# Optimization experiments

Hardware: AMD Instinct MI355X
Metric: run time of the kernel (lower is better)

## Reference

```python
import jax, jax.numpy as jnp
import numpy as np

C_IN, C_KEY, C_VAL, C_OUT = 256, 128, 128, 256
B, H, W = 4, 64, 64
BN_EPS = 1e-5


def conv1x1(x, w, b):
    # x: [B,C,H,W], w: [O,C], b: [O]
    return jnp.einsum('bchw,oc->bohw', x, w) + b[None, :, None, None]


def bn_relu(x, gamma, beta, mean, var):
    inv = jax.lax.rsqrt(var + BN_EPS)
    y = (x - mean[None, :, None, None]) * (gamma * inv)[None, :, None, None] + beta[None, :, None, None]
    return jax.nn.relu(y)


def setup_inputs() -> dict:
    key = jax.random.key(0)
    ks = jax.random.split(key, 16)
    s = 0.05
    return {
        'x_enc': jax.random.normal(ks[0], (B, C_IN, H, W), jnp.float32),
        'x_dec': jax.random.normal(ks[1], (B, C_IN, H, W), jnp.float32),
        # f_key: conv + BN params
        'wk': jax.random.normal(ks[2], (C_KEY, C_IN), jnp.float32) * s,
        'bk': jax.random.normal(ks[3], (C_KEY,), jnp.float32) * s,
        'gk': jax.random.uniform(ks[4], (C_KEY,), jnp.float32, 0.5, 1.5),
        'betak': jax.random.normal(ks[5], (C_KEY,), jnp.float32) * s,
        'mk': jax.random.normal(ks[6], (C_KEY,), jnp.float32) * s,
        'vk': jax.random.uniform(ks[7], (C_KEY,), jnp.float32, 0.5, 1.5),
        # f_query: conv + BN params
        'wq': jax.random.normal(ks[8], (C_KEY, C_IN), jnp.float32) * s,
        'bq': jax.random.normal(ks[9], (C_KEY,), jnp.float32) * s,
        'gq': jax.random.uniform(ks[10], (C_KEY,), jnp.float32, 0.5, 1.5),
        'betaq': jax.random.normal(ks[11], (C_KEY,), jnp.float32) * s,
        'mq': jax.random.normal(ks[12], (C_KEY,), jnp.float32) * s,
        'vq': jax.random.uniform(ks[13], (C_KEY,), jnp.float32, 0.5, 1.5),
        # f_value conv
        'wv': jax.random.normal(ks[14], (C_VAL, C_IN), jnp.float32) * s,
        'bv': jnp.zeros((C_VAL,), jnp.float32),
        # output projection W (random instead of zero-init to avoid degenerate baseline)
        'wo': jax.random.normal(ks[15], (C_OUT, C_VAL), jnp.float32) * s,
        'bo': jnp.zeros((C_OUT,), jnp.float32),
    }


def reference(x_enc, x_dec, wk, bk, gk, betak, mk, vk, wq, bq, gq, betaq, mq, vq, wv, bv, wo, bo):
    b, _, h, w = x_enc.shape
    hw = h * w
    # value: [B, HW, Cv]
    value = conv1x1(x_enc, wv, bv).reshape(b, C_VAL, hw).transpose(0, 2, 1)
    # query: [B, HW, Ck]
    query = bn_relu(conv1x1(x_dec, wq, bq), gq, betaq, mq, vq).reshape(b, C_KEY, hw).transpose(0, 2, 1)
    # key: [B, Ck, HW]
    key = bn_relu(conv1x1(x_enc, wk, bk), gk, betak, mk, vk).reshape(b, C_KEY, hw)
    sim = jnp.einsum('bqc,bck->bqk', query, key) * (C_KEY ** -0.5)  # [B, HW, HW]
    attn = jax.nn.softmax(sim, axis=-1)
    context = jnp.einsum('bqk,bkc->bqc', attn, value)  # [B, HW, Cv]
    context = context.transpose(0, 2, 1).reshape(b, C_VAL, h, w)
    return conv1x1(context, wo, bo)
```

## Files before the change

kernel.cpp:

```cpp
#include <hip/hip_runtime.h>

typedef __attribute__((ext_vector_type(8))) short short8;
typedef __attribute__((ext_vector_type(4))) float floatx4;

#define HW 4096
#define CIN 256
#define CK 128
#define COUT 256
#define NB 4
#define BN_EPS 1e-5f
#define SC2 0.12751744526f

#define MFMA(a, b, c) __builtin_amdgcn_mfma_f32_16x16x32_bf16((a), (b), (c), 0, 0, 0)

__device__ __forceinline__ unsigned short f2bf(float f) {
  union { float f; unsigned u; } v; v.f = f;
  unsigned r = v.u + 0x7fffu + ((v.u >> 16) & 1u);
  return (unsigned short)(r >> 16);
}

__device__ __forceinline__ short8 pack8(const float* p) {
  short8 r;
#pragma unroll
  for (int i = 0; i < 8; ++i) r[i] = (short)f2bf(p[i]);
  return r;
}

__global__ __launch_bounds__(256) void proj_kernel(
    const float* __restrict__ x_enc, const float* __restrict__ x_dec,
    const float* __restrict__ wq, const float* __restrict__ bq,
    const float* __restrict__ gq, const float* __restrict__ betaq,
    const float* __restrict__ mq, const float* __restrict__ vq,
    const float* __restrict__ wk, const float* __restrict__ bk,
    const float* __restrict__ gk, const float* __restrict__ betak,
    const float* __restrict__ mk, const float* __restrict__ vk,
    const float* __restrict__ wv, const float* __restrict__ bv,
    unsigned short* __restrict__ Qb, unsigned short* __restrict__ Kb,
    unsigned short* __restrict__ Vt)
{
  const int tid = threadIdx.x;
  const int pt = blockIdx.x;
  const int b  = blockIdx.y;
  const int pj = blockIdx.z;

  const float* X = (pj == 0) ? x_dec : x_enc;
  const float* W = (pj == 0) ? wq : (pj == 1 ? wk : wv);

  __shared__ float xF[64 * 68];
  __shared__ unsigned short xT[64 * 264];

  const float* Xs = X + (size_t)b * CIN * HW + (size_t)pt * 64;
#pragma unroll
  for (int qtr = 0; qtr < 4; ++qtr) {
    if (qtr) __syncthreads();
    {
      const int c = tid >> 2;
      const int p0 = (tid & 3) * 16;
      const float* src = Xs + (size_t)(qtr * 64 + c) * HW + p0;
#pragma unroll
      for (int j = 0; j < 4; ++j)
        *(float4*)&xF[c * 68 + p0 + j * 4] = *(const float4*)(src + j * 4);
    }
    __syncthreads();
    {
      const int p = tid & 63;
      const int cb = tid >> 6;
#pragma unroll
      for (int jj = 0; jj < 2; ++jj) {
        const int c0 = (jj * 4 + cb) * 8;
        float t[8];
#pragma unroll
        for (int u = 0; u < 8; ++u) t[u] = xF[(c0 + u) * 68 + p];
        *(short8*)&xT[p * 264 + qtr * 64 + c0] = pack8(t);
      }
    }
  }
  __syncthreads();

  const int wave = tid >> 6;
  const int lane = tid & 63;
  const int lane16 = lane & 15;
  const int quad = lane >> 4;

  floatx4 acc[2][4];
#pragma unroll
  for (int mt = 0; mt < 2; ++mt)
#pragma unroll
    for (int nf = 0; nf < 4; ++nf) acc[mt][nf] = (floatx4){0.f, 0.f, 0.f, 0.f};

#pragma unroll
  for (int ks = 0; ks < 8; ++ks) {
    short8 af[2];
#pragma unroll
    for (int mt = 0; mt < 2; ++mt) {
      const int o = wave * 32 + mt * 16 + lane16;
      const float* Wr = W + (size_t)o * CIN + ks * 32 + quad * 8;
      float t[8];
      *(float4*)(t) = *(const float4*)(Wr);
      *(float4*)(t + 4) = *(const float4*)(Wr + 4);
      af[mt] = pack8(t);
    }
#pragma unroll
    for (int nf = 0; nf < 4; ++nf) {
      const short8 bf = *(const short8*)&xT[(nf * 16 + lane16) * 264 + ks * 32 + quad * 8];
#pragma unroll
      for (int mt = 0; mt < 2; ++mt) acc[mt][nf] = MFMA(af[mt], bf, acc[mt][nf]);
    }
  }

  if (pj == 2) {
#pragma unroll
    for (int mt = 0; mt < 2; ++mt) {
#pragma unroll
      for (int r = 0; r < 4; ++r) {
        const int c = wave * 32 + mt * 16 + quad * 4 + r;
        const float bias = bv[c];
        unsigned short* dst = Vt + ((size_t)(b * CK + c)) * HW + pt * 64;
#pragma unroll
        for (int nf = 0; nf < 4; ++nf)
          dst[nf * 16 + lane16] = f2bf(acc[mt][nf][r] + bias);
      }
    }
  } else {
    const float* bias  = pj ? bk : bq;
    const float* gamma = pj ? gk : gq;
    const float* beta  = pj ? betak : betaq;
    const float* mean  = pj ? mk : mq;
    const float* var   = pj ? vk : vq;
    const float qs     = pj ? 1.f : SC2;
    unsigned short* Out = pj ? Kb : Qb;
    float sc[2][4], off[2][4];
#pragma unroll
    for (int mt = 0; mt < 2; ++mt)
#pragma unroll
      for (int r = 0; r < 4; ++r) {
        const int o = wave * 32 + mt * 16 + quad * 4 + r;
        const float s = gamma[o] * rsqrtf(var[o] + BN_EPS) * qs;
        sc[mt][r] = s;
        off[mt][r] = (bias[o] - mean[o]) * s + beta[o] * qs;
      }
#pragma unroll
    for (int nf = 0; nf < 4; ++nf) {
      const size_t prow = ((size_t)b * HW + pt * 64 + nf * 16 + lane16) * CK;
#pragma unroll
      for (int mt = 0; mt < 2; ++mt) {
        ushort4 pk;
        pk.x = f2bf(fmaxf(acc[mt][nf][0] * sc[mt][0] + off[mt][0], 0.f));
        pk.y = f2bf(fmaxf(acc[mt][nf][1] * sc[mt][1] + off[mt][1], 0.f));
        pk.z = f2bf(fmaxf(acc[mt][nf][2] * sc[mt][2] + off[mt][2], 0.f));
        pk.w = f2bf(fmaxf(acc[mt][nf][3] * sc[mt][3] + off[mt][3], 0.f));
        *(ushort4*)(Out + prow + wave * 32 + mt * 16 + quad * 4) = pk;
      }
    }
  }
}

template<int NKC>
__global__ __launch_bounds__(256, 2) void attn_kernel3(
    const unsigned short* __restrict__ Qb, const unsigned short* __restrict__ Kb,
    const unsigned short* __restrict__ Vt, float* __restrict__ Opart,
    float* __restrict__ Ml)
{
  constexpr int ITERS = 64 / NKC;
  const int tid = threadIdx.x;
  const int blk = blockIdx.x;
  const int b  = blk & 3;
  const int qt = (blk >> 2) & 31;
  const int kc = blk >> 7;

  const int wave = tid >> 6;
  const int lane = tid & 63;
  const int lane16 = lane & 15;
  const int quad = lane >> 4;

  __shared__ unsigned short Kl[64 * 136];
  __shared__ unsigned short Vl[128 * 72];
  __shared__ unsigned short Pl[4][32 * 72];
  unsigned short* Pw = &Pl[wave][0];

  const int q0 = qt * 128 + wave * 32;
  short8 qf[2][4];
  {
    const unsigned short* Qs = Qb + ((size_t)b * HW + q0) * CK;
#pragma unroll
    for (int mt = 0; mt < 2; ++mt)
#pragma unroll
      for (int ks = 0; ks < 4; ++ks)
        qf[mt][ks] = *(const short8*)(Qs + (size_t)(mt * 16 + lane16) * CK + ks * 32 + quad * 8);
  }

  short8 ones;
#pragma unroll
  for (int i = 0; i < 8; ++i) ones[i] = (short)0x3F80;

  floatx4 O[2][8];
  floatx4 Lacc[2];
#pragma unroll
  for (int mt = 0; mt < 2; ++mt) {
    Lacc[mt] = (floatx4){0.f, 0.f, 0.f, 0.f};
#pragma unroll
    for (int nf = 0; nf < 8; ++nf) O[mt][nf] = (floatx4){0.f, 0.f, 0.f, 0.f};
  }

  const unsigned short* Kg0 = Kb + (size_t)b * HW * CK;
  const unsigned short* Vg0 = Vt + (size_t)b * CK * HW;

  const int krow = tid >> 4;
  const int kcol = (tid & 15) * 8;
  const int vrow = tid >> 1;
  const int vcol = (tid & 1) * 32;

  for (int it = 0; it < ITERS; ++it) {
    const int kp0 = kc * (ITERS * 64) + it * 64;
    __syncthreads();
    {
      const unsigned short* Kg = Kg0 + (size_t)kp0 * CK;
      short8 kr[4], vr[4];
#pragma unroll
      for (int i2 = 0; i2 < 4; ++i2)
        kr[i2] = *(const short8*)(Kg + (size_t)(krow + i2 * 16) * CK + kcol);
      const unsigned short* Vg = Vg0 + (size_t)vrow * HW + kp0 + vcol;
#pragma unroll
      for (int i2 = 0; i2 < 4; ++i2)
        vr[i2] = *(const short8*)(Vg + i2 * 8);
#pragma unroll
      for (int i2 = 0; i2 < 4; ++i2)
        *(short8*)&Kl[(krow + i2 * 16) * 136 + kcol] = kr[i2];
#pragma unroll
      for (int i2 = 0; i2 < 4; ++i2)
        *(short8*)&Vl[vrow * 72 + vcol + i2 * 8] = vr[i2];
    }
    __syncthreads();

#pragma unroll
    for (int nf = 0; nf < 4; ++nf) {
      floatx4 s0 = (floatx4){0.f, 0.f, 0.f, 0.f};
      floatx4 s1 = (floatx4){0.f, 0.f, 0.f, 0.f};
#pragma unroll
      for (int ks = 0; ks < 4; ++ks) {
        const short8 kf = *(const short8*)&Kl[(nf * 16 + lane16) * 136 + ks * 32 + quad * 8];
        s0 = MFMA(qf[0][ks], kf, s0);
        s1 = MFMA(qf[1][ks], kf, s1);
      }
#pragma unroll
      for (int r = 0; r < 4; ++r) {
        Pw[(quad * 4 + r) * 72 + nf * 16 + lane16] =
            f2bf(__builtin_amdgcn_exp2f(s0[r]));
        Pw[(16 + quad * 4 + r) * 72 + nf * 16 + lane16] =
            f2bf(__builtin_amdgcn_exp2f(s1[r]));
      }
    }
    __threadfence_block();

#pragma unroll
    for (int ks = 0; ks < 2; ++ks) {
      const short8 pf0 = *(const short8*)&Pw[lane16 * 72 + ks * 32 + quad * 8];
      const short8 pf1 = *(const short8*)&Pw[(16 + lane16) * 72 + ks * 32 + quad * 8];
      Lacc[0] = MFMA(pf0, ones, Lacc[0]);
      Lacc[1] = MFMA(pf1, ones, Lacc[1]);
#pragma unroll
      for (int nf = 0; nf < 8; ++nf) {
        const short8 vf = *(const short8*)&Vl[(nf * 16 + lane16) * 72 + ks * 32 + quad * 8];
        O[0][nf] = MFMA(pf0, vf, O[0][nf]);
        O[1][nf] = MFMA(pf1, vf, O[1][nf]);
      }
    }
  }

  const int chunk = (b * 32 + qt) * NKC + kc;
  float* Op = Opart + (size_t)chunk * (128 * 128);
#pragma unroll
  for (int mt = 0; mt < 2; ++mt)
#pragma unroll
    for (int nf = 0; nf < 8; ++nf)
#pragma unroll
      for (int r = 0; r < 4; ++r)
        Op[(size_t)(wave * 32 + mt * 16 + quad * 4 + r) * 128 + nf * 16 + lane16] = O[mt][nf][r];
  if (lane16 == 0) {
    float* Mp = Ml + (size_t)chunk * 128 + wave * 32;
#pragma unroll
    for (int mt = 0; mt < 2; ++mt)
#pragma unroll
      for (int r = 0; r < 4; ++r)
        Mp[mt * 16 + quad * 4 + r] = Lacc[mt][r];
  }
}

template<int NKC>
__global__ __launch_bounds__(256) void combine_kernel(
    const float* __restrict__ Opart, const float* __restrict__ Ml,
    unsigned short* __restrict__ ctx)
{
  const int tid = threadIdx.x;
  const int blk = blockIdx.x;
  const int b  = blk >> 7;
  const int qg = blk & 127;
  const int qt = qg >> 2;
  const int qin = (qg & 3) * 32 + (tid >> 3);
  const int c16 = (tid & 7) * 16;

  const int chunk0 = (b * 32 + qt) * NKC;
  float L = 0.f;
#pragma unroll
  for (int k = 0; k < NKC; ++k) L += Ml[(size_t)(chunk0 + k) * 128 + qin];

  float acc[16];
#pragma unroll
  for (int i = 0; i < 16; ++i) acc[i] = 0.f;
#pragma unroll
  for (int k = 0; k < NKC; ++k) {
    const float* Op = Opart + (size_t)(chunk0 + k) * 16384 + (size_t)qin * 128 + c16;
#pragma unroll
    for (int j = 0; j < 4; ++j) {
      const float4 v = *(const float4*)(Op + j * 4);
      acc[j * 4 + 0] += v.x;
      acc[j * 4 + 1] += v.y;
      acc[j * 4 + 2] += v.z;
      acc[j * 4 + 3] += v.w;
    }
  }
  const float inv = 1.f / L;
  unsigned short* Cs = ctx + ((size_t)b * HW + qg * 32 + (tid >> 3)) * CK + c16;
#pragma unroll
  for (int i = 0; i < 16; ++i) Cs[i] = f2bf(acc[i] * inv);
}

__global__ __launch_bounds__(256) void outproj_kernel(
    const unsigned short* __restrict__ ctx, const float* __restrict__ wo,
    const float* __restrict__ bo, float* __restrict__ out)
{
  const int tid = threadIdx.x;
  const int pt = blockIdx.x;
  const int b  = blockIdx.y;
  const int wave = tid >> 6;
  const int lane = tid & 63;
  const int lane16 = lane & 15;
  const int quad = lane >> 4;

  floatx4 acc[4][4];
#pragma unroll
  for (int mt = 0; mt < 4; ++mt)
#pragma unroll
    for (int nf = 0; nf < 4; ++nf) acc[mt][nf] = (floatx4){0.f, 0.f, 0.f, 0.f};

#pragma unroll
  for (int ks = 0; ks < 4; ++ks) {
    short8 af[4];
#pragma unroll
    for (int mt = 0; mt < 4; ++mt) {
      const int o = wave * 64 + mt * 16 + lane16;
      const float* Wr = wo + (size_t)o * CK + ks * 32 + quad * 8;
      float t[8];
      *(float4*)(t) = *(const float4*)(Wr);
      *(float4*)(t + 4) = *(const float4*)(Wr + 4);
      af[mt] = pack8(t);
    }
#pragma unroll
    for (int nf = 0; nf < 4; ++nf) {
      const short8 bf = *(const short8*)(ctx + ((size_t)b * HW + pt * 64 + nf * 16 + lane16) * CK + ks * 32 + quad * 8);
#pragma unroll
      for (int mt = 0; mt < 4; ++mt) acc[mt][nf] = MFMA(af[mt], bf, acc[mt][nf]);
    }
  }

#pragma unroll
  for (int mt = 0; mt < 4; ++mt) {
#pragma unroll
    for (int r = 0; r < 4; ++r) {
      const int o = wave * 64 + mt * 16 + quad * 4 + r;
      const float bias = bo[o];
      float* dst = out + ((size_t)b * COUT + o) * HW + pt * 64;
#pragma unroll
      for (int nf = 0; nf < 4; ++nf)
        dst[nf * 16 + lane16] = acc[mt][nf][r] + bias;
    }
  }
}

extern "C" void kernel_launch(void* const* d_in, const int* in_sizes, int n_in,
                              void* d_out, int out_size, void* d_ws, size_t ws_size,
                              hipStream_t stream)
{
  (void)in_sizes; (void)n_in; (void)out_size;
  const float* x_enc = (const float*)d_in[0];
  const float* x_dec = (const float*)d_in[1];
  const float* wk    = (const float*)d_in[2];
  const float* bk    = (const float*)d_in[3];
  const float* gk    = (const float*)d_in[4];
  const float* betak = (const float*)d_in[5];
  const float* mk    = (const float*)d_in[6];
  const float* vk    = (const float*)d_in[7];
  const float* wq    = (const float*)d_in[8];
  const float* bq    = (const float*)d_in[9];
  const float* gq    = (const float*)d_in[10];
  const float* betaq = (const float*)d_in[11];
  const float* mq    = (const float*)d_in[12];
  const float* vq    = (const float*)d_in[13];
  const float* wv    = (const float*)d_in[14];
  const float* bv    = (const float*)d_in[15];
  const float* wo    = (const float*)d_in[16];
  const float* bo    = (const float*)d_in[17];
  float* out = (float*)d_out;

  const size_t qkv = (size_t)NB * HW * CK;
  unsigned short* Qb  = (unsigned short*)d_ws;
  unsigned short* Kb  = Qb + qkv;
  unsigned short* Vt  = Kb + qkv;
  unsigned short* ctx = Vt + qkv;
  float* Opart = (float*)(ctx + qkv);
  const size_t bf16_bytes = 4 * qkv * 2;

  proj_kernel<<<dim3(64, 4, 3), 256, 0, stream>>>(
      x_enc, x_dec, wq, bq, gq, betaq, mq, vq,
      wk, bk, gk, betak, mk, vk, wv, bv, Qb, Kb, Vt);

  auto need = [&](int nkc) {
    return bf16_bytes + (size_t)128 * nkc * (16384 + 128) * sizeof(float);
  };
  if (ws_size >= need(4)) {
    float* Ml = Opart + (size_t)128 * 4 * 16384;
    attn_kernel3<4><<<dim3(512), 256, 0, stream>>>(Qb, Kb, Vt, Opart, Ml);
    combine_kernel<4><<<dim3(512), 256, 0, stream>>>(Opart, Ml, ctx);
  } else if (ws_size >= need(2)) {
    float* Ml = Opart + (size_t)128 * 2 * 16384;
    attn_kernel3<2><<<dim3(256), 256, 0, stream>>>(Qb, Kb, Vt, Opart, Ml);
    combine_kernel<2><<<dim3(512), 256, 0, stream>>>(Opart, Ml, ctx);
  } else {
    float* Ml = Opart + (size_t)128 * 1 * 16384;
    attn_kernel3<1><<<dim3(128), 256, 0, stream>>>(Qb, Kb, Vt, Opart, Ml);
    combine_kernel<1><<<dim3(512), 256, 0, stream>>>(Opart, Ml, ctx);
  }

  outproj_kernel<<<dim3(64, 4), 256, 0, stream>>>(ctx, wo, bo, out);
}
```

Before: 189.8 us.

## Fuse K/V projections, prefetch K/V tiles in attention, fold combine into outproj

The projection kernel now computes K and V in one block that shares the staged x_enc tile, so x_enc is loaded and transposed once instead of twice. The attention kernel loads the next K/V tile into registers while the current tile is computed, overlapping global loads with MFMA work. The combine kernel is removed: the output projection sums the partial Opart chunks and normalises by L on the fly, which drops one launch and the bf16 ctx round trip. The risks are higher register pressure from the prefetch and the larger accumulator, and the output projection now redundantly rereading fp32 partials across its blocks.

Measured after the change: 192.5 us. No clear change (+1.4%).

```diff
diff --git a/kernel.cpp b/kernel.cpp
--- a/kernel.cpp
+++ b/kernel.cpp
@@ -44,7 +44,6 @@
   const int pj = blockIdx.z;
 
   const float* X = (pj == 0) ? x_dec : x_enc;
-  const float* W = (pj == 0) ? wq : (pj == 1 ? wk : wv);
 
   __shared__ float xF[64 * 68];
   __shared__ unsigned short xT[64 * 264];
@@ -82,62 +81,42 @@
   const int lane16 = lane & 15;
   const int quad = lane >> 4;
 
-  floatx4 acc[2][4];
-#pragma unroll
-  for (int mt = 0; mt < 2; ++mt)
-#pragma unroll
-    for (int nf = 0; nf < 4; ++nf) acc[mt][nf] = (floatx4){0.f, 0.f, 0.f, 0.f};
-
-#pragma unroll
-  for (int ks = 0; ks < 8; ++ks) {
-    short8 af[2];
-#pragma unroll
-    for (int mt = 0; mt < 2; ++mt) {
-      const int o = wave * 32 + mt * 16 + lane16;
-      const float* Wr = W + (size_t)o * CIN + ks * 32 + quad * 8;
-      float t[8];
-      *(float4*)(t) = *(const float4*)(Wr);
-      *(float4*)(t + 4) = *(const float4*)(Wr + 4);
-      af[mt] = pack8(t);
-    }
-#pragma unroll
-    for (int nf = 0; nf < 4; ++nf) {
-      const short8 bf = *(const short8*)&xT[(nf * 16 + lane16) * 264 + ks * 32 + quad * 8];
-#pragma unroll
-      for (int mt = 0; mt < 2; ++mt) acc[mt][nf] = MFMA(af[mt], bf, acc[mt][nf]);
-    }
-  }
-
-  if (pj == 2) {
-#pragma unroll
-    for (int mt = 0; mt < 2; ++mt) {
-#pragma unroll
-      for (int r = 0; r < 4; ++r) {
-        const int c = wave * 32 + mt * 16 + quad * 4 + r;
-        const float bias = bv[c];
-        unsigned short* dst = Vt + ((size_t)(b * CK + c)) * HW + pt * 64;
-#pragma unroll
-        for (int nf = 0; nf < 4; ++nf)
-          dst[nf * 16 + lane16] = f2bf(acc[mt][nf][r] + bias);
-      }
-    }
-  } else {
-    const float* bias  = pj ? bk : bq;
-    const float* gamma = pj ? gk : gq;
-    const float* beta  = pj ? betak : betaq;
-    const float* mean  = pj ? mk : mq;
-    const float* var   = pj ? vk : vq;
-    const float qs     = pj ? 1.f : SC2;
-    unsigned short* Out = pj ? Kb : Qb;
+  if (pj == 0) {
+    floatx4 acc[2][4];
+#pragma unroll
+    for (int mt = 0; mt < 2; ++mt)
+#pragma unroll
+      for (int nf = 0; nf < 4; ++nf) acc[mt][nf] = (floatx4){0.f, 0.f, 0.f, 0.f};
+
+#pragma unroll
+    for (int ks = 0; ks < 8; ++ks) {
+      short8 af[2];
+#pragma unroll
+      for (int mt = 0; mt < 2; ++mt) {
+        const int o = wave * 32 + mt * 16 + lane16;
+        const float* Wr = wq + (size_t)o * CIN + ks * 32 + quad * 8;
+        float t[8];
+        *(float4*)(t) = *(const float4*)(Wr);
+        *(float4*)(t + 4) = *(const float4*)(Wr + 4);
+        af[mt] = pack8(t);
+      }
+#pragma unroll
+      for (int nf = 0; nf < 4; ++nf) {
+        const short8 bf = *(const short8*)&xT[(nf * 16 + lane16) * 264 + ks * 32 + quad * 8];
+#pragma unroll
+        for (int mt = 0; mt < 2; ++mt) acc[mt][nf] = MFMA(af[mt], bf, acc[mt][nf]);
+      }
+    }
+
     float sc[2][4], off[2][4];
 #pragma unroll
     for (int mt = 0; mt < 2; ++mt)
 #pragma unroll
       for (int r = 0; r < 4; ++r) {
         const int o = wave * 32 + mt * 16 + quad * 4 + r;
-        const float s = gamma[o] * rsqrtf(var[o] + BN_EPS) * qs;
+        const float s = gq[o] * rsqrtf(vq[o] + BN_EPS) * SC2;
         sc[mt][r] = s;
-        off[mt][r] = (bias[o] - mean[o]) * s + beta[o] * qs;
+        off[mt][r] = (bq[o] - mq[o]) * s + betaq[o] * SC2;
       }
 #pragma unroll
     for (int nf = 0; nf < 4; ++nf) {
@@ -149,14 +128,81 @@
         pk.y = f2bf(fmaxf(acc[mt][nf][1] * sc[mt][1] + off[mt][1], 0.f));
         pk.z = f2bf(fmaxf(acc[mt][nf][2] * sc[mt][2] + off[mt][2], 0.f));
         pk.w = f2bf(fmaxf(acc[mt][nf][3] * sc[mt][3] + off[mt][3], 0.f));
-        *(ushort4*)(Out + prow + wave * 32 + mt * 16 + quad * 4) = pk;
+        *(ushort4*)(Qb + prow + wave * 32 + mt * 16 + quad * 4) = pk;
+      }
+    }
+  } else {
+    const bool isK = (wave < 2);
+    floatx4 acc[4][4];
+#pragma unroll
+    for (int mt = 0; mt < 4; ++mt)
+#pragma unroll
+      for (int nf = 0; nf < 4; ++nf) acc[mt][nf] = (floatx4){0.f, 0.f, 0.f, 0.f};
+
+#pragma unroll
+    for (int ks = 0; ks < 8; ++ks) {
+      short8 af[4];
+#pragma unroll
+      for (int mt = 0; mt < 4; ++mt) {
+        const int o = wave * 64 + mt * 16 + lane16;
+        const float* Wr = (isK ? wk + (size_t)o * CIN
+                               : wv + (size_t)(o - 128) * CIN) + ks * 32 + quad * 8;
+        float t[8];
+        *(float4*)(t) = *(const float4*)(Wr);
+        *(float4*)(t + 4) = *(const float4*)(Wr + 4);
+        af[mt] = pack8(t);
+      }
+#pragma unroll
+      for (int nf = 0; nf < 4; ++nf) {
+        const short8 bf = *(const short8*)&xT[(nf * 16 + lane16) * 264 + ks * 32 + quad * 8];
+#pragma unroll
+        for (int mt = 0; mt < 4; ++mt) acc[mt][nf] = MFMA(af[mt], bf, acc[mt][nf]);
+      }
+    }
+
+    if (isK) {
+      float sc[4][4], off[4][4];
+#pragma unroll
+      for (int mt = 0; mt < 4; ++mt)
+#pragma unroll
+        for (int r = 0; r < 4; ++r) {
+          const int o = wave * 64 + mt * 16 + quad * 4 + r;
+          const float s = gk[o] * rsqrtf(vk[o] + BN_EPS);
+          sc[mt][r] = s;
+          off[mt][r] = (bk[o] - mk[o]) * s + betak[o];
+        }
+#pragma unroll
+      for (int nf = 0; nf < 4; ++nf) {
+        const size_t prow = ((size_t)b * HW + pt * 64 + nf * 16 + lane16) * CK;
+#pragma unroll
+        for (int mt = 0; mt < 4; ++mt) {
+          ushort4 pk;
+          pk.x = f2bf(fmaxf(acc[mt][nf][0] * sc[mt][0] + off[mt][0], 0.f));
+          pk.y = f2bf(fmaxf(acc[mt][nf][1] * sc[mt][1] + off[mt][1], 0.f));
+          pk.z = f2bf(fmaxf(acc[mt][nf][2] * sc[mt][2] + off[mt][2], 0.f));
+          pk.w = f2bf(fmaxf(acc[mt][nf][3] * sc[mt][3] + off[mt][3], 0.f));
+          *(ushort4*)(Kb + prow + wave * 64 + mt * 16 + quad * 4) = pk;
+        }
+      }
+    } else {
+#pragma unroll
+      for (int mt = 0; mt < 4; ++mt) {
+#pragma unroll
+        for (int r = 0; r < 4; ++r) {
+          const int c = wave * 64 + mt * 16 + quad * 4 + r - 128;
+          const float bias = bv[c];
+          unsigned short* dst = Vt + ((size_t)(b * CK + c)) * HW + pt * 64;
+#pragma unroll
+          for (int nf = 0; nf < 4; ++nf)
+            dst[nf * 16 + lane16] = f2bf(acc[mt][nf][r] + bias);
+        }
       }
     }
   }
 }
 
 template<int NKC>
-__global__ __launch_bounds__(256, 2) void attn_kernel3(
+__global__ __launch_bounds__(256, 2) void attn_kernel4(
     const unsigned short* __restrict__ Qb, const unsigned short* __restrict__ Kb,
     const unsigned short* __restrict__ Vt, float* __restrict__ Opart,
     float* __restrict__ Ml)
@@ -202,35 +248,42 @@
     for (int nf = 0; nf < 8; ++nf) O[mt][nf] = (floatx4){0.f, 0.f, 0.f, 0.f};
   }
 
-  const unsigned short* Kg0 = Kb + (size_t)b * HW * CK;
-  const unsigned short* Vg0 = Vt + (size_t)b * CK * HW;
-
   const int krow = tid >> 4;
   const int kcol = (tid & 15) * 8;
   const int vrow = tid >> 1;
   const int vcol = (tid & 1) * 32;
 
+  const unsigned short* Kg = Kb + (size_t)b * HW * CK + (size_t)(kc * ITERS * 64) * CK;
+  const unsigned short* Vg = Vt + (size_t)b * CK * HW + kc * ITERS * 64;
+
+  short8 kr[4], vr[4];
+#pragma unroll
+  for (int i2 = 0; i2 < 4; ++i2)
+    kr[i2] = *(const short8*)(Kg + (size_t)(krow + i2 * 16) * CK + kcol);
+#pragma unroll
+  for (int i2 = 0; i2 < 4; ++i2)
+    vr[i2] = *(const short8*)(Vg + (size_t)vrow * HW + vcol + i2 * 8);
+
   for (int it = 0; it < ITERS; ++it) {
-    const int kp0 = kc * (ITERS * 64) + it * 64;
     __syncthreads();
-    {
-      const unsigned short* Kg = Kg0 + (size_t)kp0 * CK;
-      short8 kr[4], vr[4];
+#pragma unroll
+    for (int i2 = 0; i2 < 4; ++i2)
+      *(short8*)&Kl[(krow + i2 * 16) * 136 + kcol] = kr[i2];
+#pragma unroll
+    for (int i2 = 0; i2 < 4; ++i2)
+      *(short8*)&Vl[vrow * 72 + vcol + i2 * 8] = vr[i2];
+    __syncthreads();
+
+    if (it + 1 < ITERS) {
+      const unsigned short* Kn = Kg + (size_t)((it + 1) * 64) * CK;
+      const unsigned short* Vn = Vg + (it + 1) * 64;
 #pragma unroll
       for (int i2 = 0; i2 < 4; ++i2)
-        kr[i2] = *(const short8*)(Kg + (size_t)(krow + i2 * 16) * CK + kcol);
-      const unsigned short* Vg = Vg0 + (size_t)vrow * HW + kp0 + vcol;
+        kr[i2] = *(const short8*)(Kn + (size_t)(krow + i2 * 16) * CK + kcol);
 #pragma unroll
       for (int i2 = 0; i2 < 4; ++i2)
-        vr[i2] = *(const short8*)(Vg + i2 * 8);
-#pragma unroll
-      for (int i2 = 0; i2 < 4; ++i2)
-        *(short8*)&Kl[(krow + i2 * 16) * 136 + kcol] = kr[i2];
-#pragma unroll
-      for (int i2 = 0; i2 < 4; ++i2)
-        *(short8*)&Vl[vrow * 72 + vcol + i2 * 8] = vr[i2];
-    }
-    __syncthreads();
+        vr[i2] = *(const short8*)(Vn + (size_t)vrow * HW + vcol + i2 * 8);
+    }
 
 #pragma unroll
     for (int nf = 0; nf < 4; ++nf) {
@@ -287,47 +340,10 @@
 }
 
 template<int NKC>
-__global__ __launch_bounds__(256) void combine_kernel(
+__global__ __launch_bounds__(256) void outproj_kernel(
     const float* __restrict__ Opart, const float* __restrict__ Ml,
-    unsigned short* __restrict__ ctx)
-{
-  const int tid = threadIdx.x;
-  const int blk = blockIdx.x;
-  const int b  = blk >> 7;
-  const int qg = blk & 127;
-  const int qt = qg >> 2;
-  const int qin = (qg & 3) * 32 + (tid >> 3);
-  const int c16 = (tid & 7) * 16;
-
-  const int chunk0 = (b * 32 + qt) * NKC;
-  float L = 0.f;
-#pragma unroll
-  for (int k = 0; k < NKC; ++k) L += Ml[(size_t)(chunk0 + k) * 128 + qin];
-
-  float acc[16];
-#pragma unroll
-  for (int i = 0; i < 16; ++i) acc[i] = 0.f;
-#pragma unroll
-  for (int k = 0; k < NKC; ++k) {
-    const float* Op = Opart + (size_t)(chunk0 + k) * 16384 + (size_t)qin * 128 + c16;
-#pragma unroll
-    for (int j = 0; j < 4; ++j) {
-      const float4 v = *(const float4*)(Op + j * 4);
-      acc[j * 4 + 0] += v.x;
-      acc[j * 4 + 1] += v.y;
-      acc[j * 4 + 2] += v.z;
-      acc[j * 4 + 3] += v.w;
-    }
-  }
-  const float inv = 1.f / L;
-  unsigned short* Cs = ctx + ((size_t)b * HW + qg * 32 + (tid >> 3)) * CK + c16;
-#pragma unroll
-  for (int i = 0; i < 16; ++i) Cs[i] = f2bf(acc[i] * inv);
-}
-
-__global__ __launch_bounds__(256) void outproj_kernel(
-    const unsigned short* __restrict__ ctx, const float* __restrict__ wo,
-    const float* __restrict__ bo, float* __restrict__ out)
+    const float* __restrict__ wo, const float* __restrict__ bo,
+    float* __restrict__ out)
 {
   const int tid = threadIdx.x;
   const int pt = blockIdx.x;
@@ -337,11 +353,25 @@
   const int lane16 = lane & 15;
   const int quad = lane >> 4;
 
-  floatx4 acc[4][4];
+  const int qt = pt >> 2;
+  const int q0 = (pt & 3) * 32;
+  const int chunk0 = (b * 32 + qt) * NKC;
+
+  float invl[2];
+#pragma unroll
+  for (int nf = 0; nf < 2; ++nf) {
+    const int qrow = q0 + nf * 16 + lane16;
+    float L = 0.f;
+#pragma unroll
+    for (int k = 0; k < NKC; ++k) L += Ml[(size_t)(chunk0 + k) * 128 + qrow];
+    invl[nf] = 1.f / L;
+  }
+
+  floatx4 acc[4][2];
 #pragma unroll
   for (int mt = 0; mt < 4; ++mt)
 #pragma unroll
-    for (int nf = 0; nf < 4; ++nf) acc[mt][nf] = (floatx4){0.f, 0.f, 0.f, 0.f};
+    for (int nf = 0; nf < 2; ++nf) acc[mt][nf] = (floatx4){0.f, 0.f, 0.f, 0.f};
 
 #pragma unroll
   for (int ks = 0; ks < 4; ++ks) {
@@ -356,8 +386,23 @@
       af[mt] = pack8(t);
     }
 #pragma unroll
-    for (int nf = 0; nf < 4; ++nf) {
-      const short8 bf = *(const short8*)(ctx + ((size_t)b * HW + pt * 64 + nf * 16 + lane16) * CK + ks * 32 + quad * 8);
+    for (int nf = 0; nf < 2; ++nf) {
+      const int qrow = q0 + nf * 16 + lane16;
+      const float* Op = Opart + (size_t)chunk0 * 16384 + (size_t)qrow * 128 + ks * 32 + quad * 8;
+      float t[8];
+#pragma unroll
+      for (int u = 0; u < 8; ++u) t[u] = 0.f;
+#pragma unroll
+      for (int k = 0; k < NKC; ++k) {
+        const float4 v0 = *(const float4*)(Op + (size_t)k * 16384);
+        const float4 v1 = *(const float4*)(Op + (size_t)k * 16384 + 4);
+        t[0] += v0.x; t[1] += v0.y; t[2] += v0.z; t[3] += v0.w;
+        t[4] += v1.x; t[5] += v1.y; t[6] += v1.z; t[7] += v1.w;
+      }
+      const float iv = invl[nf];
+#pragma unroll
+      for (int u = 0; u < 8; ++u) t[u] *= iv;
+      const short8 bf = pack8(t);
 #pragma unroll
       for (int mt = 0; mt < 4; ++mt) acc[mt][nf] = MFMA(af[mt], bf, acc[mt][nf]);
     }
@@ -369,9 +414,9 @@
     for (int r = 0; r < 4; ++r) {
       const int o = wave * 64 + mt * 16 + quad * 4 + r;
       const float bias = bo[o];
-      float* dst = out + ((size_t)b * COUT + o) * HW + pt * 64;
-#pragma unroll
-      for (int nf = 0; nf < 4; ++nf)
+      float* dst = out + ((size_t)b * COUT + o) * HW + qt * 128 + q0;
+#pragma unroll
+      for (int nf = 0; nf < 2; ++nf)
         dst[nf * 16 + lane16] = acc[mt][nf][r] + bias;
     }
   }
@@ -403,14 +448,13 @@
   float* out = (float*)d_out;
 
   const size_t qkv = (size_t)NB * HW * CK;
-  unsigned short* Qb  = (unsigned short*)d_ws;
-  unsigned short* Kb  = Qb + qkv;
-  unsigned short* Vt  = Kb + qkv;
-  unsigned short* ctx = Vt + qkv;
-  float* Opart = (float*)(ctx + qkv);
-  const size_t bf16_bytes = 4 * qkv * 2;
-
-  proj_kernel<<<dim3(64, 4, 3), 256, 0, stream>>>(
+  unsigned short* Qb = (unsigned short*)d_ws;
+  unsigned short* Kb = Qb + qkv;
+  unsigned short* Vt = Kb + qkv;
+  float* Opart = (float*)(Vt + qkv);
+  const size_t bf16_bytes = 3 * qkv * 2;
+
+  proj_kernel<<<dim3(64, 4, 2), 256, 0, stream>>>(
       x_enc, x_dec, wq, bq, gq, betaq, mq, vq,
       wk, bk, gk, betak, mk, vk, wv, bv, Qb, Kb, Vt);
 
@@ -419,17 +463,15 @@
   };
   if (ws_size >= need(4)) {
     float* Ml = Opart + (size_t)128 * 4 * 16384;
-    attn_kernel3<4><<<dim3(512), 256, 0, stream>>>(Qb, Kb, Vt, Opart, Ml);
-    combine_kernel<4><<<dim3(512), 256, 0, stream>>>(Opart, Ml, ctx);
+    attn_kernel4<4><<<dim3(512), 256, 0, stream>>>(Qb, Kb, Vt, Opart, Ml);
+    outproj_kernel<4><<<dim3(128, 4), 256, 0, stream>>>(Opart, Ml, wo, bo, out);
   } else if (ws_size >= need(2)) {
     float* Ml = Opart + (size_t)128 * 2 * 16384;
-    attn_kernel3<2><<<dim3(256), 256, 0, stream>>>(Qb, Kb, Vt, Opart, Ml);
-    combine_kernel<2><<<dim3(512), 256, 0, stream>>>(Opart, Ml, ctx);
+    attn_kernel4<2><<<dim3(256), 256, 0, stream>>>(Qb, Kb, Vt, Opart, Ml);
+    outproj_kernel<2><<<dim3(128, 4), 256, 0, stream>>>(Opart, Ml, wo, bo, out);
   } else {
     float* Ml = Opart + (size_t)128 * 1 * 16384;
-    attn_kernel3<1><<<dim3(128), 256, 0, stream>>>(Qb, Kb, Vt, Opart, Ml);
-    combine_kernel<1><<<dim3(512), 256, 0, stream>>>(Opart, Ml, ctx);
-  }
-
-  outproj_kernel<<<dim3(64, 4), 256, 0, stream>>>(ctx, wo, bo, out);
-}
+    attn_kernel4<1><<<dim3(128), 256, 0, stream>>>(Qb, Kb, Vt, Opart, Ml);
+    outproj_kernel<1><<<dim3(128, 4), 256, 0, stream>>>(Opart, Ml, wo, bo, out);
+  }
+}
```
